# Kernel tuning notes

Hardware: AMD Instinct MI355X
Metric: run time of the kernel (lower is better)

## Reference

```python
import jax, jax.numpy as jnp
import numpy as np

DIM = 1024
HEADS = 16
RADIUS = 4


def setup_inputs() -> dict:
    key = jax.random.key(0)
    ks = jax.random.split(key, 5)
    B, T, D = 4, 2048, DIM
    s = 1.0 / np.sqrt(D)
    x = jax.random.normal(ks[0], (B, T, D), dtype=jnp.float32)
    w_qkv = jax.random.uniform(ks[1], (3 * D, D), minval=-s, maxval=s, dtype=jnp.float32)
    b_qkv = jax.random.uniform(ks[2], (3 * D,), minval=-s, maxval=s, dtype=jnp.float32)
    w_proj = jax.random.uniform(ks[3], (D, D), minval=-s, maxval=s, dtype=jnp.float32)
    b_proj = jax.random.uniform(ks[4], (D,), minval=-s, maxval=s, dtype=jnp.float32)
    return {"x": x, "w_qkv": w_qkv, "b_qkv": b_qkv, "w_proj": w_proj, "b_proj": b_proj}


def reference(x, w_qkv, b_qkv, w_proj, b_proj):
    B, T, D = x.shape
    H = HEADS
    hd = D // H
    scale = hd ** -0.5
    qkv = x @ w_qkv.T + b_qkv                       # [B,T,3D]
    qkv = qkv.reshape(B, T, 3, H, hd).transpose(2, 0, 3, 1, 4)  # [3,B,H,T,hd]
    q, k, v = qkv[0], qkv[1], qkv[2]
    attn = jnp.einsum('bhqd,bhkd->bhqk', q, k) * scale  # [B,H,T,T]
    idx = jnp.arange(T)
    mask = jnp.abs(idx[None, :] - idx[:, None]) > RADIUS  # [T,T]
    attn = jnp.where(mask[None, None], -jnp.inf, attn)
    attn = jax.nn.softmax(attn, axis=-1)
    out = jnp.einsum('bhqk,bhkd->bhqd', attn, v)    # [B,H,T,hd]
    out = out.transpose(0, 2, 1, 3).reshape(B, T, D)
    return out @ w_proj.T + b_proj
```

## Files before the change

kernel.cpp:

```cpp
#include <hip/hip_runtime.h>
#include <hip/hip_bf16.h>
#include <cstdint>
#include <cstddef>
#include <type_traits>


typedef __hip_bfloat16 bf16;
typedef __attribute__((ext_vector_type(8))) short bf16x8;
typedef __attribute__((ext_vector_type(4))) float f32x4;
typedef __attribute__((ext_vector_type(8))) unsigned short u16x8;

#define BATCH  4
#define SEQ    2048
#define DIM    1024
#define NHEAD  16
#define HDIM   64
#define RADIUS 4
#define ROWS   (BATCH * SEQ)
#define KDIM   1024

__device__ __forceinline__ void async_copy16(const void* gptr, void* lptr) {
    __builtin_amdgcn_global_load_lds(
        (const __attribute__((address_space(1))) unsigned int*)(uintptr_t)gptr,
        (__attribute__((address_space(3))) unsigned int*)(uint32_t)(uintptr_t)lptr,
        16, 0, 0);
}

__global__ __launch_bounds__(256)
void cvt_all(const float* __restrict__ s1, bf16* __restrict__ d1, int n1,
             const float* __restrict__ s2, bf16* __restrict__ d2, int n2,
             const float* __restrict__ s3, bf16* __restrict__ d3, int n3) {
    int i = blockIdx.x * blockDim.x + threadIdx.x;
    const float* src; bf16* dst;
    if (i < n1)              { src = s1; dst = d1; }
    else if (i < n1 + n2)    { i -= n1; src = s2; dst = d2; }
    else if (i < n1+n2+n3)   { i -= n1 + n2; src = s3; dst = d3; }
    else return;
    const float4 a = ((const float4*)src)[2 * i];
    const float4 b = ((const float4*)src)[2 * i + 1];
    union { u16x8 v; __hip_bfloat16 h[8]; } o;
    o.h[0] = __float2bfloat16(a.x); o.h[1] = __float2bfloat16(a.y);
    o.h[2] = __float2bfloat16(a.z); o.h[3] = __float2bfloat16(a.w);
    o.h[4] = __float2bfloat16(b.x); o.h[5] = __float2bfloat16(b.y);
    o.h[6] = __float2bfloat16(b.z); o.h[7] = __float2bfloat16(b.w);
    ((u16x8*)dst)[i] = o.v;
}

template <int NMAT, typename OutT>
__global__ __launch_bounds__(256)
void gemm_bt_bias(const bf16* __restrict__ A, const bf16* __restrict__ B,
                  const float* __restrict__ bias, OutT* __restrict__ C) {
    __shared__ bf16 As[128 * 64];
    __shared__ bf16 Bs[128 * 64];

    const int tid  = threadIdx.x;
    const int lane = tid & 63;
    const int wave = tid >> 6;
    const int quad = lane >> 4;
    const int l16  = lane & 15;

    const int tileM = blockIdx.y * 128;
    const int tileN = blockIdx.x * 128;
    const int wm = (wave >> 1) * 64;
    const int wn = (wave & 1) * 64;

    f32x4 acc[4][4] = {};

    for (int kt = 0; kt < KDIM; kt += 64) {
        #pragma unroll
        for (int i = 0; i < 4; ++i) {
            const int c   = i * 256 + tid;
            const int row = c >> 3;
            const int kg  = (c & 7) ^ (row & 7);
            async_copy16(A + (size_t)(tileM + row) * KDIM + kt + kg * 8,
                         (char*)As + c * 16);
            async_copy16(B + (size_t)(tileN + row) * KDIM + kt + kg * 8,
                         (char*)Bs + c * 16);
        }
        __syncthreads();

        #pragma unroll
        for (int ks = 0; ks < 2; ++ks) {
            const int kq = ks * 4 + quad;
            const int so = (kq ^ (l16 & 7)) * 8;
            bf16x8 aF[4], bF[4];
            #pragma unroll
            for (int mt = 0; mt < 4; ++mt)
                aF[mt] = *(const bf16x8*)(As + (wm + mt * 16 + l16) * 64 + so);
            #pragma unroll
            for (int nt = 0; nt < 4; ++nt)
                bF[nt] = *(const bf16x8*)(Bs + (wn + nt * 16 + l16) * 64 + so);

            #pragma unroll
            for (int mt = 0; mt < 4; ++mt)
                #pragma unroll
                for (int nt = 0; nt < 4; ++nt)
                    acc[mt][nt] = __builtin_amdgcn_mfma_f32_16x16x32_bf16(
                        aF[mt], bF[nt], acc[mt][nt], 0, 0, 0);
        }
        __syncthreads();
    }

    #pragma unroll
    for (int nt = 0; nt < 4; ++nt) {
        const int col = tileN + wn + nt * 16 + l16;
        const float bv = bias[col];
        #pragma unroll
        for (int mt = 0; mt < 4; ++mt) {
            #pragma unroll
            for (int r = 0; r < 4; ++r) {
                const int rowg = tileM + wm + mt * 16 + quad * 4 + r;
                const float v = acc[mt][nt][r] + bv;
                if constexpr (std::is_same<OutT, float>::value)
                    C[(size_t)rowg * NMAT + col] = v;
                else
                    C[(size_t)rowg * NMAT + col] = __float2bfloat16(v);
            }
        }
    }
}

__device__ __forceinline__ void bf8_to_f32(const uint4 u, float* f) {
    union { uint32_t u; float f; } c;
    c.u = u.x << 16;         f[0] = c.f;
    c.u = u.x & 0xffff0000u; f[1] = c.f;
    c.u = u.y << 16;         f[2] = c.f;
    c.u = u.y & 0xffff0000u; f[3] = c.f;
    c.u = u.z << 16;         f[4] = c.f;
    c.u = u.z & 0xffff0000u; f[5] = c.f;
    c.u = u.w << 16;         f[6] = c.f;
    c.u = u.w & 0xffff0000u; f[7] = c.f;
}

__global__ __launch_bounds__(256)
void attn_banded2(const bf16* __restrict__ qkv, bf16* __restrict__ aout) {
    const int tid = threadIdx.x;
    const int qi  = tid >> 1;
    const int hf  = tid & 1;
    const int t0  = blockIdx.x * 128;
    const int h   = blockIdx.y;
    const int b   = blockIdx.z;
    const int t   = t0 + qi;

    const size_t rowstride = 3072;
    const size_t base = ((size_t)b * SEQ + t) * rowstride + h * HDIM + hf * 32;
    const float scale = 0.125f;

    float q32[32];
    {
        const uint4* qp = (const uint4*)(qkv + base);
        uint4 u0 = qp[0], u1 = qp[1], u2 = qp[2], u3 = qp[3];
        bf8_to_f32(u0, q32 + 0);  bf8_to_f32(u1, q32 + 8);
        bf8_to_f32(u2, q32 + 16); bf8_to_f32(u3, q32 + 24);
    }

    float sc[2 * RADIUS + 1];
    #pragma unroll
    for (int j = 0; j < 2 * RADIUS + 1; ++j) {
        const int k = t - RADIUS + j;
        const bool valid = (k >= 0) && (k < SEQ);
        const int kc = valid ? k : t;
        const uint4* kp = (const uint4*)(qkv + base + ((size_t)(kc - t)) * rowstride + 1024);
        float kf[32];
        uint4 u0 = kp[0], u1 = kp[1], u2 = kp[2], u3 = kp[3];
        bf8_to_f32(u0, kf + 0);  bf8_to_f32(u1, kf + 8);
        bf8_to_f32(u2, kf + 16); bf8_to_f32(u3, kf + 24);
        float p = 0.f;
        #pragma unroll
        for (int e = 0; e < 32; ++e) p = fmaf(q32[e], kf[e], p);
        p += __shfl_xor(p, 1, 64);
        sc[j] = valid ? p * scale : -1e30f;
    }

    float mx = sc[0];
    #pragma unroll
    for (int j = 1; j < 2 * RADIUS + 1; ++j) mx = fmaxf(mx, sc[j]);
    float sum = 0.f;
    #pragma unroll
    for (int j = 0; j < 2 * RADIUS + 1; ++j) { sc[j] = __expf(sc[j] - mx); sum += sc[j]; }
    const float inv = 1.0f / sum;

    float o32[32];
    #pragma unroll
    for (int e = 0; e < 32; ++e) o32[e] = 0.f;
    #pragma unroll
    for (int j = 0; j < 2 * RADIUS + 1; ++j) {
        const int k = t - RADIUS + j;
        const int kc = (k >= 0 && k < SEQ) ? k : t;
        const uint4* vp = (const uint4*)(qkv + base + ((size_t)(kc - t)) * rowstride + 2048);
        float vf[32];
        uint4 u0 = vp[0], u1 = vp[1], u2 = vp[2], u3 = vp[3];
        bf8_to_f32(u0, vf + 0);  bf8_to_f32(u1, vf + 8);
        bf8_to_f32(u2, vf + 16); bf8_to_f32(u3, vf + 24);
        const float w = sc[j];
        #pragma unroll
        for (int e = 0; e < 32; ++e) o32[e] = fmaf(w, vf[e], o32[e]);
    }

    bf16* op = aout + ((size_t)b * SEQ + t) * DIM + h * HDIM + hf * 32;
    #pragma unroll
    for (int c = 0; c < 4; ++c) {
        union { u16x8 v; __hip_bfloat16 hh[8]; } o;
        #pragma unroll
        for (int e = 0; e < 8; ++e) o.hh[e] = __float2bfloat16(o32[c * 8 + e] * inv);
        ((u16x8*)op)[c] = o.v;
    }
}

extern "C" void kernel_launch(void* const* d_in, const int* in_sizes, int n_in,
                              void* d_out, int out_size, void* d_ws, size_t ws_size,
                              hipStream_t stream) {
    const float* x      = (const float*)d_in[0];
    const float* w_qkv  = (const float*)d_in[1];
    const float* b_qkv  = (const float*)d_in[2];
    const float* w_proj = (const float*)d_in[3];
    const float* b_proj = (const float*)d_in[4];
    float* out = (float*)d_out;

    bf16* xb     = (bf16*)d_ws;
    bf16* wqkvb  = xb + (size_t)ROWS * DIM;
    bf16* wprojb = wqkvb + (size_t)3072 * 1024;
    bf16* qkvb   = wprojb + (size_t)1024 * 1024;
    bf16* attnb  = qkvb + (size_t)ROWS * 3072;

    const int n1 = ROWS * DIM / 8, n2 = 3072 * 1024 / 8, n3 = 1024 * 1024 / 8;
    cvt_all<<<(n1 + n2 + n3 + 255) / 256, 256, 0, stream>>>(x, xb, n1, w_qkv, wqkvb, n2,
                                                            w_proj, wprojb, n3);

    gemm_bt_bias<3072, bf16><<<dim3(3072 / 128, ROWS / 128), 256, 0, stream>>>(xb, wqkvb, b_qkv, qkvb);

    attn_banded2<<<dim3(SEQ / 128, NHEAD, BATCH), 256, 0, stream>>>(qkvb, attnb);

    gemm_bt_bias<1024, float><<<dim3(1024 / 128, ROWS / 128), 256, 0, stream>>>(attnb, wprojb, b_proj, out);
}
```

Baseline: 226.0 us.

## Write QKV GEMM output in per-head [b,h,s,t,d] layout for attention

The QKV GEMM epilogue now scatters results into a head-major layout where each (batch, head, q/k/v) slice is a contiguous T×64 block. The attention kernel reads Q, K and V from these contiguous slices instead of using a 3072-element row stride. The aim is better locality and coalescing for the banded attention loads. In exchange, the GEMM epilogue does extra index arithmetic, and its stores stay strided per 16 columns.

```diff
diff --git a/kernel.cpp b/kernel.cpp
--- a/kernel.cpp
+++ b/kernel.cpp
@@ -18,6 +18,7 @@
 #define RADIUS 4
 #define ROWS   (BATCH * SEQ)
 #define KDIM   1024
+#define HSLICE (SEQ * HDIM)
 
 __device__ __forceinline__ void async_copy16(const void* gptr, void* lptr) {
     __builtin_amdgcn_global_load_lds(
@@ -46,7 +47,7 @@
     ((u16x8*)dst)[i] = o.v;
 }
 
-template <int NMAT, typename OutT>
+template <int NMAT, typename OutT, bool QKV_LAYOUT>
 __global__ __launch_bounds__(256)
 void gemm_bt_bias(const bf16* __restrict__ A, const bf16* __restrict__ B,
                   const float* __restrict__ bias, OutT* __restrict__ C) {
@@ -103,18 +104,27 @@
 
     #pragma unroll
     for (int nt = 0; nt < 4; ++nt) {
-        const int col = tileN + wn + nt * 16 + l16;
-        const float bv = bias[col];
+        const int scol = tileN + wn + nt * 16;
+        const float bv = bias[scol + l16];
         #pragma unroll
         for (int mt = 0; mt < 4; ++mt) {
             #pragma unroll
             for (int r = 0; r < 4; ++r) {
                 const int rowg = tileM + wm + mt * 16 + quad * 4 + r;
                 const float v = acc[mt][nt][r] + bv;
-                if constexpr (std::is_same<OutT, float>::value)
-                    C[(size_t)rowg * NMAT + col] = v;
-                else
-                    C[(size_t)rowg * NMAT + col] = __float2bfloat16(v);
+                if constexpr (QKV_LAYOUT) {
+                    const int s = scol >> 10;
+                    const int h = (scol >> 6) & (NHEAD - 1);
+                    const int d = (scol & 63) + l16;
+                    const int b = rowg >> 11;
+                    const int t = rowg & (SEQ - 1);
+                    ((bf16*)C)[(size_t)((b * NHEAD + h) * 3 + s) * HSLICE
+                               + (size_t)t * HDIM + d] = __float2bfloat16(v);
+                } else if constexpr (std::is_same<OutT, float>::value) {
+                    C[(size_t)rowg * NMAT + scol + l16] = v;
+                } else {
+                    C[(size_t)rowg * NMAT + scol + l16] = __float2bfloat16(v);
+                }
             }
         }
     }
@@ -133,7 +143,7 @@
 }
 
 __global__ __launch_bounds__(256)
-void attn_banded2(const bf16* __restrict__ qkv, bf16* __restrict__ aout) {
+void attn_banded3(const bf16* __restrict__ qkv, bf16* __restrict__ aout) {
     const int tid = threadIdx.x;
     const int qi  = tid >> 1;
     const int hf  = tid & 1;
@@ -142,13 +152,15 @@
     const int b   = blockIdx.z;
     const int t   = t0 + qi;
 
-    const size_t rowstride = 3072;
-    const size_t base = ((size_t)b * SEQ + t) * rowstride + h * HDIM + hf * 32;
+    const size_t bh3 = (size_t)(b * NHEAD + h) * 3;
+    const bf16* qb = qkv + (bh3 + 0) * HSLICE + (size_t)t * HDIM + hf * 32;
+    const bf16* kb = qkv + (bh3 + 1) * HSLICE + hf * 32;
+    const bf16* vb = qkv + (bh3 + 2) * HSLICE + hf * 32;
     const float scale = 0.125f;
 
     float q32[32];
     {
-        const uint4* qp = (const uint4*)(qkv + base);
+        const uint4* qp = (const uint4*)qb;
         uint4 u0 = qp[0], u1 = qp[1], u2 = qp[2], u3 = qp[3];
         bf8_to_f32(u0, q32 + 0);  bf8_to_f32(u1, q32 + 8);
         bf8_to_f32(u2, q32 + 16); bf8_to_f32(u3, q32 + 24);
@@ -160,7 +172,7 @@
         const int k = t - RADIUS + j;
         const bool valid = (k >= 0) && (k < SEQ);
         const int kc = valid ? k : t;
-        const uint4* kp = (const uint4*)(qkv + base + ((size_t)(kc - t)) * rowstride + 1024);
+        const uint4* kp = (const uint4*)(kb + (size_t)kc * HDIM);
         float kf[32];
         uint4 u0 = kp[0], u1 = kp[1], u2 = kp[2], u3 = kp[3];
         bf8_to_f32(u0, kf + 0);  bf8_to_f32(u1, kf + 8);
@@ -187,7 +199,7 @@
     for (int j = 0; j < 2 * RADIUS + 1; ++j) {
         const int k = t - RADIUS + j;
         const int kc = (k >= 0 && k < SEQ) ? k : t;
-        const uint4* vp = (const uint4*)(qkv + base + ((size_t)(kc - t)) * rowstride + 2048);
+        const uint4* vp = (const uint4*)(vb + (size_t)kc * HDIM);
         float vf[32];
         uint4 u0 = vp[0], u1 = vp[1], u2 = vp[2], u3 = vp[3];
         bf8_to_f32(u0, vf + 0);  bf8_to_f32(u1, vf + 8);
@@ -227,9 +239,11 @@
     cvt_all<<<(n1 + n2 + n3 + 255) / 256, 256, 0, stream>>>(x, xb, n1, w_qkv, wqkvb, n2,
                                                             w_proj, wprojb, n3);
 
-    gemm_bt_bias<3072, bf16><<<dim3(3072 / 128, ROWS / 128), 256, 0, stream>>>(xb, wqkvb, b_qkv, qkvb);
-
-    attn_banded2<<<dim3(SEQ / 128, NHEAD, BATCH), 256, 0, stream>>>(qkvb, attnb);
-
-    gemm_bt_bias<1024, float><<<dim3(1024 / 128, ROWS / 128), 256, 0, stream>>>(attnb, wprojb, b_proj, out);
-}
+    gemm_bt_bias<3072, bf16, true><<<dim3(3072 / 128, ROWS / 128), 256, 0, stream>>>(
+        xb, wqkvb, b_qkv, qkvb);
+
+    attn_banded3<<<dim3(SEQ / 128, NHEAD, BATCH), 256, 0, stream>>>(qkvb, attnb);
+
+    gemm_bt_bias<1024, float, false><<<dim3(1024 / 128, ROWS / 128), 256, 0, stream>>>(
+        attnb, wprojb, b_proj, out);
+}
```

Measured after the change: 222.8 us. Within noise of the previous version (-1.4%).
